# Kernel optimization log

Hardware: AMD Instinct MI355X
Metric: run time of the kernel (lower is better)

Reference implementation:

```python
import jax, jax.numpy as jnp
import numpy as np

N, D, K = 100000, 512, 32
H1, H2 = 512, 256
LN2PI_2 = float(np.log(2.0 * np.pi) / 2.0)


def _glorot(key, shape):
    fan_in, fan_out = shape[0], shape[1]
    limit = np.sqrt(6.0 / (fan_in + fan_out))
    return jax.random.uniform(key, shape, jnp.float32, -limit, limit)


def setup_inputs() -> dict:
    key = jax.random.key(0)
    k0, k1, k2, k3 = jax.random.split(key, 4)
    return {
        "x": jax.random.normal(k0, (N, D), jnp.float32),
        "W1": _glorot(k1, (D, H1)),
        "b1": jnp.zeros((H1,), jnp.float32),
        "W2": _glorot(k2, (H1, H2)),
        "b2": jnp.zeros((H2,), jnp.float32),
        "W3": _glorot(k3, (H2, K)),
        "b3": jnp.zeros((K,), jnp.float32),
    }


def reference(x, W1, b1, W2, b2, W3, b3):
    # instance attention MLP: softplus hiddens, softmax output -> [N, K]
    h = jax.nn.softplus(x @ W1 + b1)
    h = jax.nn.softplus(h @ W2 + b2)
    att = jax.nn.softmax(h @ W3 + b3, axis=-1)

    att_sum = jnp.sum(att, axis=0)  # [K]
    # weighted mean: sum_n x[n,d] * att[n,k] / sum_n att[n,k]  -> [K, D]
    means = (att.T @ x) / att_sum[:, None]
    # weighted variance: E_w[x^2] - mean^2 (algebraic expansion of
    # sum_n (x - mean)^2 * att / sum att, avoids [N,K,D] intermediate)
    ex2 = (att.T @ (x * x)) / att_sum[:, None]  # [K, D]
    vars_ = ex2 - means * means

    # GMM diagonal log-likelihood, expanded to GEMM form:
    inv_v = 1.0 / vars_  # [K, D]
    maha = (x * x) @ inv_v.T - 2.0 * (x @ (means * inv_v).T) \
           + jnp.sum(means * means * inv_v, axis=-1)[None, :]  # [N, K]
    gmm_log = -0.5 * maha - 0.5 * jnp.sum(jnp.log(vars_), axis=-1)[None, :] - D * LN2PI_2
    return gmm_log, vars_
```

## Files before the change

kernel.cpp:

```cpp
#include <hip/hip_runtime.h>
#include <hip/hip_bf16.h>
#include <math.h>

#define NROWS 100000
#define DDIM  512
#define KCL   32
#define H1DIM 512
#define H2DIM 256
#define LN2PI_2 0.9189385332046727f
#define NCHUNK 196
#define NPAD  100352
#define NBLKL 784
#define XBLKS 25000

typedef __attribute__((ext_vector_type(8))) short short8;
typedef __attribute__((ext_vector_type(4))) short shortx4;
typedef __attribute__((ext_vector_type(4))) float floatx4;

__device__ __forceinline__ float softplus_f(float v) {
    return fmaxf(v, 0.f) + __logf(1.f + __expf(-fabsf(v)));
}

__device__ __forceinline__ unsigned short f2bf_rne(float f) {
    unsigned int u = __float_as_uint(f);
    return (unsigned short)((u + 0x7fffu + ((u >> 16) & 1u)) >> 16);
}

__device__ __forceinline__ float bf2f(short v) {
    return __uint_as_float(((unsigned int)(unsigned short)v) << 16);
}

__global__ __launch_bounds__(256) void cvt_all(
    const float* __restrict__ x, short* __restrict__ xb,
    const float* __restrict__ W1, const float* __restrict__ W2,
    const float* __restrict__ W3, short* __restrict__ W1T,
    short* __restrict__ W2T, short* __restrict__ W3T)
{
    const int b = blockIdx.x;
    if (b < XBLKS) {
        size_t i = ((size_t)b * 256 + threadIdx.x) * 8;
        float4 f0 = *(const float4*)&x[i];
        float4 f1 = *(const float4*)&x[i + 4];
        short8 o;
        o[0] = (short)f2bf_rne(f0.x); o[1] = (short)f2bf_rne(f0.y);
        o[2] = (short)f2bf_rne(f0.z); o[3] = (short)f2bf_rne(f0.w);
        o[4] = (short)f2bf_rne(f1.x); o[5] = (short)f2bf_rne(f1.y);
        o[6] = (short)f2bf_rne(f1.z); o[7] = (short)f2bf_rne(f1.w);
        *(short8*)&xb[i] = o;
        return;
    }
    int idx = (b - XBLKS) * 256 + threadIdx.x;
    const int n1 = DDIM * H1DIM;
    const int n2 = H1DIM * H2DIM;
    const int n3 = H2DIM * KCL;
    if (idx < n1) {
        int n = idx % H1DIM, k = idx / H1DIM;
        W1T[(size_t)n * DDIM + k] = (short)f2bf_rne(W1[idx]);
    } else if (idx < n1 + n2) {
        int rel = idx - n1;
        int n = rel % H2DIM, k = rel / H2DIM;
        W2T[(size_t)n * H1DIM + k] = (short)f2bf_rne(W2[rel]);
    } else if (idx < n1 + n2 + n3) {
        int rel = idx - n1 - n2;
        int n = rel % KCL, k = rel / KCL;
        W3T[(size_t)n * H2DIM + k] = (short)f2bf_rne(W3[rel]);
    }
}

#define LDP 40
__global__ __launch_bounds__(512) void gemm_sp(
    const short* __restrict__ A, const short* __restrict__ BT,
    const float* __restrict__ bias, short* __restrict__ Cptr,
    int M, int Nc, int Kd)
{
    __shared__ short As[2][128 * LDP];
    __shared__ short Bs[2][256 * LDP];

    const int tid = threadIdx.x;
    const int lid = tid & 63;
    const int w = tid >> 6;
    const int lm = lid & 15;
    const int lq = lid >> 4;
    const int wrow = (w & 1) * 64;
    const int wcol = (w >> 1) * 64;

    const int row0 = blockIdx.y * 128;
    const int col0 = blockIdx.x * 256;

    const int sr = tid >> 2;
    const int sc = (tid & 3) << 3;

    int gr = row0 + sr; if (gr >= M) gr = M - 1;
    const short* Ar  = A + (size_t)gr * Kd + sc;
    const short* Br0 = BT + (size_t)(col0 + sr) * Kd + sc;
    const short* Br1 = BT + (size_t)(col0 + 128 + sr) * Kd + sc;

    floatx4 acc[4][4];
    #pragma unroll
    for (int i = 0; i < 4; i++)
        #pragma unroll
        for (int j = 0; j < 4; j++)
            acc[i][j] = (floatx4){0.f, 0.f, 0.f, 0.f};

    short8 pa, pb0, pb1;
    pa  = *(const short8*)Ar;
    pb0 = *(const short8*)Br0;
    pb1 = *(const short8*)Br1;

    const int nk = Kd >> 5;
    for (int kt = 0; kt < nk; kt++) {
        const int buf = kt & 1;
        *(short8*)&As[buf][sr * LDP + sc]         = pa;
        *(short8*)&Bs[buf][sr * LDP + sc]         = pb0;
        *(short8*)&Bs[buf][(128 + sr) * LDP + sc] = pb1;
        if (kt + 1 < nk) {
            int ko = (kt + 1) << 5;
            pa  = *(const short8*)(Ar + ko);
            pb0 = *(const short8*)(Br0 + ko);
            pb1 = *(const short8*)(Br1 + ko);
        }
        __syncthreads();

        short8 a[4], b[4];
        #pragma unroll
        for (int i = 0; i < 4; i++)
            a[i] = *(const short8*)&As[buf][(wrow + i * 16 + lm) * LDP + lq * 8];
        #pragma unroll
        for (int j = 0; j < 4; j++)
            b[j] = *(const short8*)&Bs[buf][(wcol + j * 16 + lm) * LDP + lq * 8];
        #pragma unroll
        for (int i = 0; i < 4; i++)
            #pragma unroll
            for (int j = 0; j < 4; j++)
                acc[i][j] = __builtin_amdgcn_mfma_f32_16x16x32_bf16(
                    a[i], b[j], acc[i][j], 0, 0, 0);
    }

    float bb[4];
    #pragma unroll
    for (int j = 0; j < 4; j++)
        bb[j] = bias[col0 + wcol + j * 16 + lm];

    #pragma unroll
    for (int i = 0; i < 4; i++) {
        #pragma unroll
        for (int reg = 0; reg < 4; reg++) {
            int rr = row0 + wrow + i * 16 + lq * 4 + reg;
            if (rr < M) {
                #pragma unroll
                for (int j = 0; j < 4; j++) {
                    int c = col0 + wcol + j * 16 + lm;
                    float v = softplus_f(acc[i][j][reg] + bb[j]);
                    Cptr[(size_t)rr * Nc + c] = (short)f2bf_rne(v);
                }
            }
        }
    }
}

__global__ __launch_bounds__(512) void gemm2_logits(
    const short* __restrict__ h1, const short* __restrict__ W2T,
    const float* __restrict__ b2, const short* __restrict__ W3T,
    const float* __restrict__ b3, short* __restrict__ attT,
    float* __restrict__ Patt)
{
    __shared__ __align__(16) short lds[32768];
    __shared__ float red[8][32];

    short* AsB = lds;
    short* BsB = lds + 2 * 128 * LDP;

    const int tid = threadIdx.x;
    const int lid = tid & 63;
    const int w = tid >> 6;
    const int lm = lid & 15;
    const int lq = lid >> 4;
    const int wrow = (w & 1) * 64;
    const int wcol = (w >> 1) * 64;

    const int row0 = blockIdx.x * 128;

    const int sr = tid >> 2;
    const int sc = (tid & 3) << 3;

    int gr = row0 + sr; if (gr >= NROWS) gr = NROWS - 1;
    const short* Ar  = h1  + (size_t)gr * H1DIM + sc;
    const short* Br0 = W2T + (size_t)sr * H1DIM + sc;
    const short* Br1 = W2T + (size_t)(128 + sr) * H1DIM + sc;

    floatx4 acc[4][4];
    #pragma unroll
    for (int i = 0; i < 4; i++)
        #pragma unroll
        for (int j = 0; j < 4; j++)
            acc[i][j] = (floatx4){0.f, 0.f, 0.f, 0.f};

    short8 pa, pb0, pb1;
    pa  = *(const short8*)Ar;
    pb0 = *(const short8*)Br0;
    pb1 = *(const short8*)Br1;

    const int nk = H1DIM >> 5;
    for (int kt = 0; kt < nk; kt++) {
        const int buf = kt & 1;
        *(short8*)&AsB[buf * (128 * LDP) + sr * LDP + sc]         = pa;
        *(short8*)&BsB[buf * (256 * LDP) + sr * LDP + sc]         = pb0;
        *(short8*)&BsB[buf * (256 * LDP) + (128 + sr) * LDP + sc] = pb1;
        if (kt + 1 < nk) {
            int ko = (kt + 1) << 5;
            pa  = *(const short8*)(Ar + ko);
            pb0 = *(const short8*)(Br0 + ko);
            pb1 = *(const short8*)(Br1 + ko);
        }
        __syncthreads();

        short8 a[4], b[4];
        #pragma unroll
        for (int i = 0; i < 4; i++)
            a[i] = *(const short8*)&AsB[buf * (128 * LDP) + (wrow + i * 16 + lm) * LDP + lq * 8];
        #pragma unroll
        for (int j = 0; j < 4; j++)
            b[j] = *(const short8*)&BsB[buf * (256 * LDP) + (wcol + j * 16 + lm) * LDP + lq * 8];
        #pragma unroll
        for (int i = 0; i < 4; i++)
            #pragma unroll
            for (int j = 0; j < 4; j++)
                acc[i][j] = __builtin_amdgcn_mfma_f32_16x16x32_bf16(
                    a[i], b[j], acc[i][j], 0, 0, 0);
    }

    __syncthreads();

    float bb2[4];
    #pragma unroll
    for (int j = 0; j < 4; j++)
        bb2[j] = b2[wcol + j * 16 + lm];
    #pragma unroll
    for (int i = 0; i < 4; i++) {
        #pragma unroll
        for (int reg = 0; reg < 4; reg++) {
            const int r = wrow + i * 16 + lq * 4 + reg;
            const int rx = (r & 7) << 4;
            #pragma unroll
            for (int j = 0; j < 4; j++) {
                const int c = wcol + j * 16 + lm;
                float v = softplus_f(acc[i][j][reg] + bb2[j]);
                *(short*)((char*)lds + ((r * 512 + c * 2) ^ rx)) =
                    (short)f2bf_rne(v);
            }
        }
    }
    __syncthreads();

    short8 bf3[2][8];
    #pragma unroll
    for (int j = 0; j < 2; j++)
        #pragma unroll
        for (int s = 0; s < 8; s++)
            bf3[j][s] = *(const short8*)&W3T[(j * 16 + lm) * H2DIM + s * 32 + lq * 8];

    floatx4 lacc[2];
    lacc[0] = (floatx4){0.f, 0.f, 0.f, 0.f};
    lacc[1] = (floatx4){0.f, 0.f, 0.f, 0.f};
    const int lr = w * 16 + lm;
    const int lrx = (lr & 7) << 4;
    #pragma unroll
    for (int s = 0; s < 8; s++) {
        short8 a0 = *(const short8*)((const char*)lds +
                        ((lr * 512 + s * 64 + lq * 16) ^ lrx));
        lacc[0] = __builtin_amdgcn_mfma_f32_16x16x32_bf16(a0, bf3[0][s], lacc[0], 0, 0, 0);
        lacc[1] = __builtin_amdgcn_mfma_f32_16x16x32_bf16(a0, bf3[1][s], lacc[1], 0, 0, 0);
    }

    const float b3v0 = b3[lm];
    const float b3v1 = b3[16 + lm];
    float p0 = 0.f, p1 = 0.f;
    float e0s[4], e1s[4];
    #pragma unroll
    for (int reg = 0; reg < 4; reg++) {
        const int rg = row0 + w * 16 + lq * 4 + reg;
        float v0 = lacc[0][reg] + b3v0;
        float v1 = lacc[1][reg] + b3v1;
        float m = fmaxf(v0, v1);
        m = fmaxf(m, __shfl_xor(m, 1));
        m = fmaxf(m, __shfl_xor(m, 2));
        m = fmaxf(m, __shfl_xor(m, 4));
        m = fmaxf(m, __shfl_xor(m, 8));
        float e0 = __expf(v0 - m);
        float e1 = __expf(v1 - m);
        float sm = e0 + e1;
        sm += __shfl_xor(sm, 1);
        sm += __shfl_xor(sm, 2);
        sm += __shfl_xor(sm, 4);
        sm += __shfl_xor(sm, 8);
        float inv = 1.f / sm;
        e0 *= inv; e1 *= inv;
        if (rg >= NROWS) { e0 = 0.f; e1 = 0.f; }
        p0 += e0; p1 += e1;
        e0s[reg] = e0; e1s[reg] = e1;
    }
    p0 += __shfl_xor(p0, 16); p0 += __shfl_xor(p0, 32);
    p1 += __shfl_xor(p1, 16); p1 += __shfl_xor(p1, 32);
    if (lq == 0) { red[w][lm] = p0; red[w][16 + lm] = p1; }

    __syncthreads();

    short (*Ts)[136] = (short(*)[136])lds;
    #pragma unroll
    for (int reg = 0; reg < 4; reg++) {
        const int rloc = w * 16 + lq * 4 + reg;
        Ts[lm][rloc]      = (short)f2bf_rne(e0s[reg]);
        Ts[16 + lm][rloc] = (short)f2bf_rne(e1s[reg]);
    }
    __syncthreads();

    if (tid < KCL) {
        float ps = 0.f;
        #pragma unroll
        for (int ww = 0; ww < 8; ww++) ps += red[ww][tid];
        Patt[blockIdx.x * KCL + tid] = ps;
    }

    {
        int rr = tid >> 4;
        int cs = (tid & 15) << 3;
        *(short8*)&attT[(size_t)rr * NPAD + row0 + cs] =
            *(const short8*)&Ts[rr][cs];
    }
}

__global__ __launch_bounds__(256, 4) void stats_mfma(
    const short* __restrict__ xb, const short* __restrict__ attT,
    float* __restrict__ P)
{
    __shared__ short xT[32 * 512];

    const int tid = threadIdx.x;
    const int lane = tid & 63;
    const int lm = lane & 15;
    const int lq = lane >> 4;
    const int w = tid >> 6;
    const int kh = w >> 1;
    const int dh = w & 1;

    const int cblk = blockIdx.x;
    const int dgrp = blockIdx.y;
    const int n0 = cblk * 512;

    short8 afrag[16];
    const short* arow = attT + (size_t)(kh * 16 + lm) * NPAD + n0 + lq * 8;
    #pragma unroll
    for (int s = 0; s < 16; s++)
        afrag[s] = *(const short8*)(arow + s * 32);

    const int c = tid & 31;
    const int rq = tid >> 5;
    const bool full = (n0 + 512 <= NROWS);

    for (int dt = 0; dt < 4; dt++) {
        const int colf = dgrp * 128 + dt * 32 + c;
        __syncthreads();
        if (full) {
            const short* xp = xb + (size_t)n0 * DDIM + colf;
            #pragma unroll 4
            for (int p = 0; p < 16; p++) {
                int rr = p * 32 + rq * 4;
                unsigned int h0 = (unsigned short)xp[(size_t)(rr + 0) * DDIM];
                unsigned int h1 = (unsigned short)xp[(size_t)(rr + 1) * DDIM];
                unsigned int h2 = (unsigned short)xp[(size_t)(rr + 2) * DDIM];
                unsigned int h3 = (unsigned short)xp[(size_t)(rr + 3) * DDIM];
                int boff = (c << 10) + ((rr * 2) ^ ((c & 15) << 4));
                *(uint2*)((char*)xT + boff) =
                    make_uint2(h0 | (h1 << 16), h2 | (h3 << 16));
            }
        } else {
            #pragma unroll 4
            for (int p = 0; p < 16; p++) {
                int rr = p * 32 + rq * 4;
                int g0 = min(n0 + rr + 0, NROWS - 1);
                int g1 = min(n0 + rr + 1, NROWS - 1);
                int g2 = min(n0 + rr + 2, NROWS - 1);
                int g3 = min(n0 + rr + 3, NROWS - 1);
                unsigned int h0 = (unsigned short)xb[(size_t)g0 * DDIM + colf];
                unsigned int h1 = (unsigned short)xb[(size_t)g1 * DDIM + colf];
                unsigned int h2 = (unsigned short)xb[(size_t)g2 * DDIM + colf];
                unsigned int h3 = (unsigned short)xb[(size_t)g3 * DDIM + colf];
                int boff = (c << 10) + ((rr * 2) ^ ((c & 15) << 4));
                *(uint2*)((char*)xT + boff) =
                    make_uint2(h0 | (h1 << 16), h2 | (h3 << 16));
            }
        }
        __syncthreads();

        floatx4 acc1 = (floatx4){0.f, 0.f, 0.f, 0.f};
        floatx4 acc2 = (floatx4){0.f, 0.f, 0.f, 0.f};
        const int rowb = (dh * 16 + lm) << 10;
        #pragma unroll
        for (int s = 0; s < 16; s++) {
            int boff = rowb + ((s * 64 + lq * 16) ^ (lm << 4));
            short8 bx = *(const short8*)((const char*)xT + boff);
            union { short8 s8; unsigned int u[4]; } bq;
            #pragma unroll
            for (int e = 0; e < 4; e++) {
                float f0 = bf2f(bx[2 * e]);
                float f1 = bf2f(bx[2 * e + 1]);
                f0 *= f0; f1 *= f1;
                bq.u[e] = (unsigned int)f2bf_rne(f0) |
                          ((unsigned int)f2bf_rne(f1) << 16);
            }
            acc1 = __builtin_amdgcn_mfma_f32_16x16x32_bf16(
                afrag[s], bx, acc1, 0, 0, 0);
            acc2 = __builtin_amdgcn_mfma_f32_16x16x32_bf16(
                afrag[s], bq.s8, acc2, 0, 0, 0);
        }

        const size_t pbase = (size_t)cblk * 32768 +
                             (size_t)(kh * 16 + lq * 4) * 512 +
                             (size_t)(dgrp * 128 + dt * 32 + dh * 16 + lm);
        #pragma unroll
        for (int reg = 0; reg < 4; reg++) {
            P[pbase + (size_t)reg * 512]         = acc1[reg];
            P[pbase + 16384 + (size_t)reg * 512] = acc2[reg];
        }
    }
}

__global__ __launch_bounds__(256) void stats_reduce(
    const float* __restrict__ P, const float* __restrict__ Patt,
    float* __restrict__ S12, float* __restrict__ att_sum)
{
    int e = blockIdx.x * 256 + threadIdx.x;
    float sum = 0.f;
    for (int cc = 0; cc < NCHUNK; cc++)
        sum += P[(size_t)cc * 32768 + e];
    S12[e] = sum;

    if (blockIdx.x == 0 && threadIdx.x < KCL) {
        float as = 0.f;
        for (int cc = 0; cc < NBLKL; cc++) as += Patt[cc * KCL + threadIdx.x];
        att_sum[threadIdx.x] = as;
    }
}

__global__ __launch_bounds__(256) void finalize_stats(
    const float* __restrict__ S12, const float* __restrict__ att_sum,
    short* __restrict__ Bp, float* __restrict__ konst,
    float* __restrict__ vars_out)
{
    int k = blockIdx.x;
    int tid = threadIdx.x;
    __shared__ float red[256];

    float inv_as = 1.f / att_sum[k];
    float csum = 0.f, lsum = 0.f;
    for (int d = tid; d < DDIM; d += 256) {
        float mean = S12[k * DDIM + d] * inv_as;
        float ex2  = S12[KCL * DDIM + k * DDIM + d] * inv_as;
        float var  = ex2 - mean * mean;
        vars_out[k * DDIM + d] = var;
        float iv = 1.f / var;
        Bp[(size_t)k * 1024 + d]       = (short)f2bf_rne(-0.5f * iv);
        Bp[(size_t)k * 1024 + 512 + d] = (short)f2bf_rne(mean * iv);
        csum += mean * mean * iv;
        lsum += logf(var);
    }
    red[tid] = csum;
    __syncthreads();
    for (int s = 128; s > 0; s >>= 1) {
        if (tid < s) red[tid] += red[tid + s];
        __syncthreads();
    }
    float ctot = red[0];
    __syncthreads();
    red[tid] = lsum;
    __syncthreads();
    for (int s = 128; s > 0; s >>= 1) {
        if (tid < s) red[tid] += red[tid + s];
        __syncthreads();
    }
    if (tid == 0)
        konst[k] = -0.5f * ctot - 0.5f * red[0] - DDIM * LN2PI_2;
}

#define LDG 40
__global__ __launch_bounds__(256) void gmm_out_mfma(
    const short* __restrict__ xb, const short* __restrict__ Bp,
    const float* __restrict__ konst, float* __restrict__ out)
{
    __shared__ short As_sq[128 * LDG];
    __shared__ short As_x[128 * LDG];

    const int tid = threadIdx.x;
    const int lane = tid & 63;
    const int lm = lane & 15;
    const int lq = lane >> 4;
    const int wid = tid >> 6;
    const int row0 = blockIdx.x * 128;

    floatx4 acc[2][2];
    #pragma unroll
    for (int i = 0; i < 2; i++)
        #pragma unroll
        for (int j = 0; j < 2; j++)
            acc[i][j] = (floatx4){0.f, 0.f, 0.f, 0.f};

    int rrh[4], segh[4], grh[4];
    bool okh[4];
    #pragma unroll
    for (int h = 0; h < 4; h++) {
        int u = tid + h * 256;
        rrh[h] = u >> 3;
        segh[h] = (u & 7) << 2;
        int gr = row0 + rrh[h];
        okh[h] = (gr < NROWS);
        grh[h] = okh[h] ? gr : 0;
    }

    shortx4 pf[4];
    #pragma unroll
    for (int h = 0; h < 4; h++) {
        shortx4 v = (shortx4){0, 0, 0, 0};
        if (okh[h]) v = *(const shortx4*)&xb[(size_t)grh[h] * DDIM + segh[h]];
        pf[h] = v;
    }

    for (int dt = 0; dt < 16; dt++) {
        __syncthreads();
        #pragma unroll
        for (int h = 0; h < 4; h++) {
            shortx4 sx = pf[h];
            shortx4 sq;
            #pragma unroll
            for (int e = 0; e < 4; e++) {
                float f = bf2f(sx[e]);
                sq[e] = (short)f2bf_rne(f * f);
            }
            *(shortx4*)&As_x[rrh[h] * LDG + segh[h]]  = sx;
            *(shortx4*)&As_sq[rrh[h] * LDG + segh[h]] = sq;
        }
        if (dt + 1 < 16) {
            #pragma unroll
            for (int h = 0; h < 4; h++) {
                shortx4 v = (shortx4){0, 0, 0, 0};
                if (okh[h])
                    v = *(const shortx4*)&xb[(size_t)grh[h] * DDIM +
                                             (dt + 1) * 32 + segh[h]];
                pf[h] = v;
            }
        }
        __syncthreads();

        short8 a_sq[2], a_x[2], b_sq[2], b_x[2];
        #pragma unroll
        for (int i = 0; i < 2; i++) {
            int off = (wid * 32 + i * 16 + lm) * LDG + lq * 8;
            a_sq[i] = *(const short8*)&As_sq[off];
            a_x[i]  = *(const short8*)&As_x[off];
        }
        #pragma unroll
        for (int j = 0; j < 2; j++) {
            const size_t bo = (size_t)(j * 16 + lm) * 1024 + dt * 32 + lq * 8;
            b_sq[j] = *(const short8*)&Bp[bo];
            b_x[j]  = *(const short8*)&Bp[bo + 512];
        }
        #pragma unroll
        for (int i = 0; i < 2; i++)
            #pragma unroll
            for (int j = 0; j < 2; j++) {
                acc[i][j] = __builtin_amdgcn_mfma_f32_16x16x32_bf16(
                    a_sq[i], b_sq[j], acc[i][j], 0, 0, 0);
                acc[i][j] = __builtin_amdgcn_mfma_f32_16x16x32_bf16(
                    a_x[i], b_x[j], acc[i][j], 0, 0, 0);
            }
    }

    float kst[2];
    kst[0] = konst[lm];
    kst[1] = konst[16 + lm];

    #pragma unroll
    for (int i = 0; i < 2; i++) {
        #pragma unroll
        for (int reg = 0; reg < 4; reg++) {
            int rr = row0 + wid * 32 + i * 16 + lq * 4 + reg;
            if (rr < NROWS) {
                out[(size_t)rr * KCL + lm]      = acc[i][0][reg] + kst[0];
                out[(size_t)rr * KCL + 16 + lm] = acc[i][1][reg] + kst[1];
            }
        }
    }
}

extern "C" void kernel_launch(void* const* d_in, const int* in_sizes, int n_in,
                              void* d_out, int out_size, void* d_ws, size_t ws_size,
                              hipStream_t stream)
{
    const float* x  = (const float*)d_in[0];
    const float* W1 = (const float*)d_in[1];
    const float* b1 = (const float*)d_in[2];
    const float* W2 = (const float*)d_in[3];
    const float* b2 = (const float*)d_in[4];
    const float* W3 = (const float*)d_in[5];
    const float* b3 = (const float*)d_in[6];
    float* out = (float*)d_out;

    short* h1b     = (short*)d_ws;
    float* h2      = (float*)(h1b + (size_t)NROWS * H1DIM);
    float* att     = h2 + (size_t)NROWS * H2DIM;
    float* P       = att + (size_t)NROWS * KCL;
    float* PattOld = P + (size_t)NCHUNK * 32768;
    float* S12     = PattOld + NCHUNK * KCL;
    float* att_sum = S12 + 2 * KCL * DDIM;
    short* Bp      = (short*)(att_sum + KCL);
    float* konst   = (float*)(Bp + KCL * 1024);
    (void)ws_size; (void)in_sizes; (void)n_in; (void)out_size; (void)PattOld;

    short* xb = (short*)h2;
    short* attT  = (short*)att;
    float* PattN = (float*)(attT + (size_t)KCL * NPAD);
    short* W1T = (short*)P;
    short* W2T = W1T + H1DIM * DDIM;
    short* W3T = W2T + H2DIM * H1DIM;

    cvt_all<<<dim3(XBLKS + 1568), 256, 0, stream>>>(
        x, xb, W1, W2, W3, W1T, W2T, W3T);

    int mblocks = (NROWS + 127) / 128;

    gemm_sp<<<dim3(H1DIM / 256, mblocks), 512, 0, stream>>>(
        xb, W1T, b1, h1b, NROWS, H1DIM, DDIM);
    gemm2_logits<<<dim3(NBLKL), 512, 0, stream>>>(
        h1b, W2T, b2, W3T, b3, attT, PattN);
    stats_mfma<<<dim3(NCHUNK, 4), 256, 0, stream>>>(xb, attT, P);
    stats_reduce<<<dim3(128), 256, 0, stream>>>(P, PattN, S12, att_sum);
    finalize_stats<<<dim3(KCL), 256, 0, stream>>>(
        S12, att_sum, Bp, konst, out + (size_t)NROWS * KCL);
    gmm_out_mfma<<<dim3(mblocks), 256, 0, stream>>>(
        xb, Bp, konst, out);
}
```

Measured before the change: 589.1 us.

## Fuse fp32-to-bf16 conversion of x into first GEMM with full-width tiles

Removes the separate conversion pass over x. The first GEMM kernel now reads fp32 x directly, converts it to bf16 with the packed v_cvt_pk_bf16_f32 instruction, stages it in shared memory and writes the bf16 copy out for later kernels. Each block now uses 1024 threads and covers all 512 output columns, so x is loaded once per row tile instead of once per column half. This cuts a full read/write pass over x. The cost is a much larger shared-memory B tile and bigger blocks, which lowers occupancy.

```diff
diff --git a/kernel.cpp b/kernel.cpp
--- a/kernel.cpp
+++ b/kernel.cpp
@@ -11,7 +11,6 @@
 #define NCHUNK 196
 #define NPAD  100352
 #define NBLKL 784
-#define XBLKS 25000
 
 typedef __attribute__((ext_vector_type(8))) short short8;
 typedef __attribute__((ext_vector_type(4))) short shortx4;
@@ -30,26 +29,21 @@
     return __uint_as_float(((unsigned int)(unsigned short)v) << 16);
 }
 
-__global__ __launch_bounds__(256) void cvt_all(
-    const float* __restrict__ x, short* __restrict__ xb,
+__device__ __forceinline__ short8 cvt8(float4 a, float4 b) {
+    union { unsigned int u[4]; short8 s; } r;
+    asm("v_cvt_pk_bf16_f32 %0, %1, %2" : "=v"(r.u[0]) : "v"(a.x), "v"(a.y));
+    asm("v_cvt_pk_bf16_f32 %0, %1, %2" : "=v"(r.u[1]) : "v"(a.z), "v"(a.w));
+    asm("v_cvt_pk_bf16_f32 %0, %1, %2" : "=v"(r.u[2]) : "v"(b.x), "v"(b.y));
+    asm("v_cvt_pk_bf16_f32 %0, %1, %2" : "=v"(r.u[3]) : "v"(b.z), "v"(b.w));
+    return r.s;
+}
+
+__global__ __launch_bounds__(256) void cvt_weights(
     const float* __restrict__ W1, const float* __restrict__ W2,
     const float* __restrict__ W3, short* __restrict__ W1T,
     short* __restrict__ W2T, short* __restrict__ W3T)
 {
-    const int b = blockIdx.x;
-    if (b < XBLKS) {
-        size_t i = ((size_t)b * 256 + threadIdx.x) * 8;
-        float4 f0 = *(const float4*)&x[i];
-        float4 f1 = *(const float4*)&x[i + 4];
-        short8 o;
-        o[0] = (short)f2bf_rne(f0.x); o[1] = (short)f2bf_rne(f0.y);
-        o[2] = (short)f2bf_rne(f0.z); o[3] = (short)f2bf_rne(f0.w);
-        o[4] = (short)f2bf_rne(f1.x); o[5] = (short)f2bf_rne(f1.y);
-        o[6] = (short)f2bf_rne(f1.z); o[7] = (short)f2bf_rne(f1.w);
-        *(short8*)&xb[i] = o;
-        return;
-    }
-    int idx = (b - XBLKS) * 256 + threadIdx.x;
+    int idx = blockIdx.x * 256 + threadIdx.x;
     const int n1 = DDIM * H1DIM;
     const int n2 = H1DIM * H2DIM;
     const int n3 = H2DIM * KCL;
@@ -68,13 +62,13 @@
 }
 
 #define LDP 40
-__global__ __launch_bounds__(512) void gemm_sp(
-    const short* __restrict__ A, const short* __restrict__ BT,
-    const float* __restrict__ bias, short* __restrict__ Cptr,
-    int M, int Nc, int Kd)
+__global__ __launch_bounds__(1024, 4) void gemm1_fused(
+    const float* __restrict__ x, const short* __restrict__ W1T,
+    const float* __restrict__ b1, short* __restrict__ h1,
+    short* __restrict__ xb)
 {
     __shared__ short As[2][128 * LDP];
-    __shared__ short Bs[2][256 * LDP];
+    __shared__ short Bs[2][512 * LDP];
 
     const int tid = threadIdx.x;
     const int lid = tid & 63;
@@ -84,16 +78,19 @@
     const int wrow = (w & 1) * 64;
     const int wcol = (w >> 1) * 64;
 
-    const int row0 = blockIdx.y * 128;
-    const int col0 = blockIdx.x * 256;
+    const int row0 = blockIdx.x * 128;
 
     const int sr = tid >> 2;
     const int sc = (tid & 3) << 3;
-
-    int gr = row0 + sr; if (gr >= M) gr = M - 1;
-    const short* Ar  = A + (size_t)gr * Kd + sc;
-    const short* Br0 = BT + (size_t)(col0 + sr) * Kd + sc;
-    const short* Br1 = BT + (size_t)(col0 + 128 + sr) * Kd + sc;
+    const bool doA = (tid < 512);
+
+    const short* Br0 = W1T + (size_t)sr * DDIM + sc;
+    const short* Br1 = W1T + (size_t)(256 + sr) * DDIM + sc;
+
+    int gra = row0 + sr;
+    if (gra >= NROWS) gra = NROWS - 1;
+    const float* Arf = x + (size_t)gra * DDIM + sc;
+    short* xbw = xb + (size_t)gra * DDIM + sc;
 
     floatx4 acc[4][4];
     #pragma unroll
@@ -102,20 +99,31 @@
         for (int j = 0; j < 4; j++)
             acc[i][j] = (floatx4){0.f, 0.f, 0.f, 0.f};
 
-    short8 pa, pb0, pb1;
-    pa  = *(const short8*)Ar;
+    float4 fa0, fa1;
+    short8 pb0, pb1;
+    if (doA) {
+        fa0 = *(const float4*)Arf;
+        fa1 = *(const float4*)(Arf + 4);
+    }
     pb0 = *(const short8*)Br0;
     pb1 = *(const short8*)Br1;
 
-    const int nk = Kd >> 5;
+    const int nk = DDIM >> 5;
     for (int kt = 0; kt < nk; kt++) {
         const int buf = kt & 1;
-        *(short8*)&As[buf][sr * LDP + sc]         = pa;
+        if (doA) {
+            short8 cv = cvt8(fa0, fa1);
+            *(short8*)&As[buf][sr * LDP + sc] = cv;
+            *(short8*)&xbw[kt * 32] = cv;
+        }
         *(short8*)&Bs[buf][sr * LDP + sc]         = pb0;
-        *(short8*)&Bs[buf][(128 + sr) * LDP + sc] = pb1;
+        *(short8*)&Bs[buf][(256 + sr) * LDP + sc] = pb1;
         if (kt + 1 < nk) {
             int ko = (kt + 1) << 5;
-            pa  = *(const short8*)(Ar + ko);
+            if (doA) {
+                fa0 = *(const float4*)(Arf + ko);
+                fa1 = *(const float4*)(Arf + ko + 4);
+            }
             pb0 = *(const short8*)(Br0 + ko);
             pb1 = *(const short8*)(Br1 + ko);
         }
@@ -139,19 +147,19 @@
     float bb[4];
     #pragma unroll
     for (int j = 0; j < 4; j++)
-        bb[j] = bias[col0 + wcol + j * 16 + lm];
+        bb[j] = b1[wcol + j * 16 + lm];
 
     #pragma unroll
     for (int i = 0; i < 4; i++) {
         #pragma unroll
         for (int reg = 0; reg < 4; reg++) {
             int rr = row0 + wrow + i * 16 + lq * 4 + reg;
-            if (rr < M) {
+            if (rr < NROWS) {
                 #pragma unroll
                 for (int j = 0; j < 4; j++) {
-                    int c = col0 + wcol + j * 16 + lm;
+                    int c = wcol + j * 16 + lm;
                     float v = softplus_f(acc[i][j][reg] + bb[j]);
-                    Cptr[(size_t)rr * Nc + c] = (short)f2bf_rne(v);
+                    h1[(size_t)rr * H1DIM + c] = (short)f2bf_rne(v);
                 }
             }
         }
@@ -622,13 +630,11 @@
     short* W2T = W1T + H1DIM * DDIM;
     short* W3T = W2T + H2DIM * H1DIM;
 
-    cvt_all<<<dim3(XBLKS + 1568), 256, 0, stream>>>(
-        x, xb, W1, W2, W3, W1T, W2T, W3T);
+    cvt_weights<<<dim3(1568), 256, 0, stream>>>(W1, W2, W3, W1T, W2T, W3T);
 
     int mblocks = (NROWS + 127) / 128;
 
-    gemm_sp<<<dim3(H1DIM / 256, mblocks), 512, 0, stream>>>(
-        xb, W1T, b1, h1b, NROWS, H1DIM, DDIM);
+    gemm1_fused<<<dim3(mblocks), 1024, 0, stream>>>(x, W1T, b1, h1b, xb);
     gemm2_logits<<<dim3(NBLKL), 512, 0, stream>>>(
         h1b, W2T, b2, W3T, b3, attT, PattN);
     stats_mfma<<<dim3(NCHUNK, 4), 256, 0, stream>>>(xb, attT, P);
```

Result: no change. 586.6 us (median of 2 runs) (-0.4%).
